# Kernel optimization log

Measured on AMD Instinct MI355X. Metric: run time of the kernel, lower is better.

## Reference

```python
import jax, jax.numpy as jnp
import numpy as np

H, CH = 4, 16          # heads, hidden_features // heads
SLOPE = 0.2            # leaky_relu negative slope


def gat(x, W, a_src, a_dst):
    # x: (B, N, C); W: (hidden, C); a_src/a_dst: (H, CH)
    B, N, _ = x.shape
    h = (x @ W.T).reshape(B, N, H, CH)
    a1 = jnp.einsum('bnhc,hc->bnh', h, a_src)   # att_src scores
    a2 = jnp.einsum('bnhc,hc->bnh', h, a_dst)   # att_dst scores
    # torch: a1.unsqueeze(1) + a2.unsqueeze(2) -> (B, N, N, H)
    e = a1[:, None, :, :] + a2[:, :, None, :]
    e = jnp.transpose(e, (0, 3, 1, 2))          # (B, H, N, N)
    e = jnp.where(e >= 0, e, SLOPE * e)         # leaky_relu
    return jax.nn.softmax(e, axis=2)            # softmax over dim=2 as in torch


def pool(x, W1, b1, W2, b2):
    # diff-pool assignment: (B, N, K), then x' = S^T x -> (B, K, C)
    s = jax.nn.softmax(jax.nn.relu(x @ W1.T + b1) @ W2.T + b2, axis=-1)
    return jnp.einsum('bnk,bnc->bkc', s, x)


def fuse(att0, atts, lefts, rights):
    out = att0
    for a, l, r in zip(atts, lefts, rights):
        # left (H,J0,K) @ att (B,H,K,K) @ right (H,K,J0), broadcast over batch
        out = out + jnp.einsum('hjk,bhkl,hlm->bhjm', l, a, r)
    return out


def setup_inputs() -> dict:
    key = jax.random.key(0)
    ks = iter(jax.random.split(key, 40))
    n = lambda shape, s=0.1: jax.random.normal(next(ks), shape, dtype=jnp.float32) * s
    inp = {
        'src': n((64, 64, 64, 25), 1.0),
        'gat_lin': n((6, 64, 64)), 'gat_asrc': n((6, 4, 16)), 'gat_adst': n((6, 4, 16)),
        'sp0_W1': n((64, 64)), 'sp0_b1': jnp.zeros((64,), jnp.float32),
        'sp0_W2': n((12, 64)), 'sp0_b2': jnp.zeros((12,), jnp.float32),
        'sp1_W1': n((64, 64)), 'sp1_b1': jnp.zeros((64,), jnp.float32),
        'sp1_W2': n((5, 64)), 'sp1_b2': jnp.zeros((5,), jnp.float32),
        'tp0_W1': n((64, 64)), 'tp0_b1': jnp.zeros((64,), jnp.float32),
        'tp0_W2': n((32, 64)), 'tp0_b2': jnp.zeros((32,), jnp.float32),
        'tp1_W1': n((64, 64)), 'tp1_b1': jnp.zeros((64,), jnp.float32),
        'tp1_W2': n((12, 64)), 'tp1_b2': jnp.zeros((12,), jnp.float32),
        'sl0': n((4, 25, 12)), 'sr0': n((4, 12, 25)),
        'sl1': n((4, 25, 5)), 'sr1': n((4, 5, 25)),
        'tl0': n((4, 64, 32)), 'tr0': n((4, 32, 64)),
        'tl1': n((4, 64, 12)), 'tr1': n((4, 12, 64)),
    }
    return inp


def reference(src, gat_lin, gat_asrc, gat_adst,
              sp0_W1, sp0_b1, sp0_W2, sp0_b2, sp1_W1, sp1_b1, sp1_W2, sp1_b2,
              tp0_W1, tp0_b1, tp0_W2, tp0_b2, tp1_W1, tp1_b1, tp1_W2, tp1_b2,
              sl0, sr0, sl1, sr1, tl0, tr0, tl1, tr1):
    B, C, T, J = src.shape
    # ---- spatial branch: attention over joints per (batch, frame) ----
    xs = jnp.transpose(src, (0, 2, 3, 1)).reshape(B * T, J, C)
    a_s0 = gat(xs, gat_lin[0], gat_asrc[0], gat_adst[0])            # (BT,H,25,25)
    xs1 = pool(xs, sp0_W1, sp0_b1, sp0_W2, sp0_b2)                  # (BT,12,C)
    a_s1 = gat(xs1, gat_lin[1], gat_asrc[1], gat_adst[1])           # (BT,H,12,12)
    xs2 = pool(xs1, sp1_W1, sp1_b1, sp1_W2, sp1_b2)                 # (BT,5,C)
    a_s2 = gat(xs2, gat_lin[2], gat_asrc[2], gat_adst[2])           # (BT,H,5,5)
    s_fused = fuse(a_s0, [a_s1, a_s2], [sl0, sl1], [sr0, sr1])
    # ---- temporal branch: attention over frames per (batch, joint) ----
    xt = jnp.transpose(src, (0, 3, 2, 1)).reshape(B * J, T, C)
    a_t0 = gat(xt, gat_lin[3], gat_asrc[3], gat_adst[3])            # (BJ,H,64,64)
    xt1 = pool(xt, tp0_W1, tp0_b1, tp0_W2, tp0_b2)                  # (BJ,32,C)
    a_t1 = gat(xt1, gat_lin[4], gat_asrc[4], gat_adst[4])
    xt2 = pool(xt1, tp1_W1, tp1_b1, tp1_W2, tp1_b2)                 # (BJ,12,C)
    a_t2 = gat(xt2, gat_lin[5], gat_asrc[5], gat_adst[5])
    t_fused = fuse(a_t0, [a_t1, a_t2], [tl0, tl1], [tr0, tr1])
    return (s_fused.reshape(B, T, H, J, J), t_fused.reshape(B, J, H, T, T))
```

## Files before the change

kernel.cpp:

```cpp
#include <hip/hip_runtime.h>

#define DEVINL __device__ __forceinline__

DEVINL float leaky(float v) { return v >= 0.f ? v : 0.2f * v; }

__global__ void wprep_kernel(const float* __restrict__ lin,
                             const float* __restrict__ asrc,
                             const float* __restrict__ adst,
                             float* __restrict__ w_out) {
    int idx = blockIdx.x * blockDim.x + threadIdx.x;
    if (idx >= 6 * 4 * 64) return;
    int c = idx & 63;
    int h = (idx >> 6) & 3;
    int k = idx >> 8;
    const float* L = lin + k * 64 * 64;
    float s1 = 0.f, s2 = 0.f;
    for (int e = 0; e < 16; ++e) {
        float w = L[(h * 16 + e) * 64 + c];
        s1 += w * asrc[(k * 4 + h) * 16 + e];
        s2 += w * adst[(k * 4 + h) * 16 + e];
    }
    w_out[(k * 2 + 0) * 256 + h * 64 + c] = s1;
    w_out[(k * 2 + 1) * 256 + h * 64 + c] = s2;
}

__global__ void wtrans_kernel(const float* __restrict__ s0, const float* __restrict__ s1,
                              const float* __restrict__ t0, const float* __restrict__ t1,
                              const float* __restrict__ s0w2, const float* __restrict__ s1w2,
                              const float* __restrict__ t0w2, const float* __restrict__ t1w2,
                              float* __restrict__ o) {
    int idx = blockIdx.x * 256 + threadIdx.x;
    if (idx < 16384) {
        int m = idx >> 12, r = idx & 4095, c = r >> 6, d = r & 63;
        const float* src = (m == 0) ? s0 : (m == 1) ? s1 : (m == 2) ? t0 : t1;
        o[idx] = src[d * 64 + c];
    } else if (idx < 16384 + 768) {
        int j = idx - 16384, c = j / 12, k = j - 12 * c;
        o[idx] = s0w2[k * 64 + c];
    } else if (idx < 17152 + 512) {
        int j = idx - 17152, c = j >> 3, k = j & 7;
        o[idx] = (k < 5) ? s1w2[k * 64 + c] : 0.f;
    } else if (idx < 17664 + 2048) {
        int j = idx - 17664, c = j >> 5, k = j & 31;
        o[idx] = t0w2[k * 64 + c];
    } else if (idx < 19712 + 768) {
        int j = idx - 19712, c = j / 12, k = j - 12 * c;
        o[idx] = t1w2[k * 64 + c];
    }
}

__global__ void xs_kernel(const float* __restrict__ src, float* __restrict__ xs) {
    int g = blockIdx.x;
    int b = g >> 6, t = g & 63;
    __shared__ float tile[64][26];
    const float* sp = src + b * 102400 + t * 25;
    for (int idx = threadIdx.x; idx < 64 * 25; idx += blockDim.x) {
        int c = idx / 25, j = idx - c * 25;
        tile[c][j] = sp[c * 1600 + j];
    }
    __syncthreads();
    float* op = xs + g * 25 * 64;
    for (int idx = threadIdx.x; idx < 25 * 64; idx += blockDim.x) {
        int j = idx >> 6, c = idx & 63;
        op[idx] = tile[c][j];
    }
}

__global__ void xt_kernel(const float* __restrict__ src, float* __restrict__ xt) {
    int g = blockIdx.x;
    int b = g / 25, j = g - b * 25;
    __shared__ float tile[64][65];
    const float* sp = src + b * 102400 + j;
    for (int idx = threadIdx.x; idx < 64 * 64; idx += blockDim.x) {
        int c = idx >> 6, t = idx & 63;
        tile[c][t] = sp[c * 1600 + t * 25];
    }
    __syncthreads();
    float* op = xt + g * 64 * 64;
    for (int idx = threadIdx.x; idx < 64 * 64; idx += blockDim.x) {
        int t = idx >> 6, c = idx & 63;
        op[idx] = tile[c][t];
    }
}

template <int N>
__global__ __launch_bounds__(256) void gat_kernel(
    const float* __restrict__ x,
    const float* __restrict__ w,
    float* __restrict__ att) {
    int g = blockIdx.x;
    const int tid = threadIdx.x;
    __shared__ float xlT[64][N + 1];
    __shared__ float wl[512];
    __shared__ float a1s[4 * N], a2s[4 * N];
    __shared__ float mxs[4];
    __shared__ float mjs[4 * N], invs[4 * N];
    const float* xp = x + (size_t)g * N * 64;
    for (int idx = tid; idx < N * 64; idx += 256) {
        int n = idx >> 6, c = idx & 63;
        xlT[c][n] = xp[idx];
    }
    for (int idx = tid; idx < 512; idx += 256) wl[idx] = w[idx];
    __syncthreads();
    for (int idx = tid; idx < 8 * N; idx += 256) {
        int n = idx % N;
        int hh = (idx / N) & 3;
        int sd = idx / (4 * N);
        const float* wp = wl + sd * 256 + hh * 64;
        float acc = 0.f;
        #pragma unroll 8
        for (int c = 0; c < 64; ++c) acc += xlT[c][n] * wp[c];
        (sd == 0 ? a1s : a2s)[hh * N + n] = acc;
    }
    __syncthreads();
    if (tid < 4) {
        float m = -1e30f;
        for (int i = 0; i < N; ++i) m = fmaxf(m, a2s[tid * N + i]);
        mxs[tid] = m;
    }
    __syncthreads();
    for (int idx = tid; idx < 4 * N; idx += 256) {
        int hh = idx / N;
        float aj = a1s[idx];
        float mj = leaky(aj + mxs[hh]);
        float ssum = 0.f;
        for (int i = 0; i < N; ++i) ssum += __expf(leaky(aj + a2s[hh * N + i]) - mj);
        mjs[idx] = mj;
        invs[idx] = 1.f / ssum;
    }
    __syncthreads();
    float* ob = att + (size_t)g * 4 * N * N;
    if constexpr ((N % 4) == 0) {
        constexpr int NF4 = N / 4;
        for (int idx = tid; idx < 4 * N * NF4; idx += 256) {
            int row = idx / NF4;
            int j0 = (idx - row * NF4) * 4;
            int hh = row / N, i = row - hh * N;
            float4 q1 = *(const float4*)&a1s[hh * N + j0];
            float4 qm = *(const float4*)&mjs[hh * N + j0];
            float4 qv = *(const float4*)&invs[hh * N + j0];
            float a2i = a2s[hh * N + i];
            float a1v[4] = {q1.x, q1.y, q1.z, q1.w};
            float mv[4] = {qm.x, qm.y, qm.z, qm.w};
            float iv[4] = {qv.x, qv.y, qv.z, qv.w};
            float r[4];
            #pragma unroll
            for (int c = 0; c < 4; ++c) {
                float e = a1v[c] + a2i;
                e = e >= 0.f ? e : 0.2f * e;
                r[c] = __expf(e - mv[c]) * iv[c];
            }
            *(float4*)&ob[row * N + j0] = make_float4(r[0], r[1], r[2], r[3]);
        }
    } else {
        for (int idx = tid; idx < 4 * N * N; idx += 256) {
            int hh = idx / (N * N), rem = idx - hh * N * N;
            int i = rem / N, j = rem - i * N;
            float e = a1s[hh * N + j] + a2s[hh * N + i];
            e = e >= 0.f ? e : 0.2f * e;
            ob[idx] = __expf(e - mjs[hh * N + j]) * invs[hh * N + j];
        }
    }
}

template <int N, int K, int KP>
__global__ __launch_bounds__(256, 3) void pool_kernel(
    const float* __restrict__ x,
    const float* __restrict__ W1T,
    const float* __restrict__ b1,
    const float* __restrict__ W2T,
    const float* __restrict__ b2,
    float* __restrict__ xo) {
    constexpr int NP = (N + 3) & ~3;
    constexpr int LDN = NP + 1;
    __shared__ float xlT[64 * LDN];
    __shared__ float yT[64 * LDN];
    __shared__ float sT[KP * LDN];
    const int g = blockIdx.x, tid = threadIdx.x;
    const float* xp = x + (size_t)g * N * 64;
    for (int i4 = tid; i4 < N * 16; i4 += 256) {
        int n = i4 >> 4, c0 = (i4 & 15) << 2;
        float4 v = ((const float4*)xp)[i4];
        xlT[(c0 + 0) * LDN + n] = v.x;
        xlT[(c0 + 1) * LDN + n] = v.y;
        xlT[(c0 + 2) * LDN + n] = v.z;
        xlT[(c0 + 3) * LDN + n] = v.w;
    }
    if constexpr (NP > N) {
        for (int i = tid; i < 64 * (NP - N); i += 256) {
            int c = i / (NP - N), n = N + i % (NP - N);
            xlT[c * LDN + n] = 0.f;
        }
    }
    __syncthreads();
    constexpr int T1 = (NP / 4) * 16;
    if (tid < T1) {
        int d0 = (tid & 15) << 2, n0 = (tid >> 4) << 2;
        float acc[4][4] = {};
        #pragma unroll 4
        for (int c = 0; c < 64; ++c) {
            float4 w4 = *(const float4*)(W1T + c * 64 + d0);
            float wv[4] = {w4.x, w4.y, w4.z, w4.w};
            float xv[4];
            #pragma unroll
            for (int r = 0; r < 4; ++r) xv[r] = xlT[c * LDN + n0 + r];
            #pragma unroll
            for (int r = 0; r < 4; ++r)
                #pragma unroll
                for (int cc = 0; cc < 4; ++cc) acc[r][cc] += xv[r] * wv[cc];
        }
        float4 b4 = *(const float4*)(b1 + d0);
        float bb[4] = {b4.x, b4.y, b4.z, b4.w};
        #pragma unroll
        for (int r = 0; r < 4; ++r)
            #pragma unroll
            for (int cc = 0; cc < 4; ++cc)
                yT[(d0 + cc) * LDN + n0 + r] = fmaxf(acc[r][cc] + bb[cc], 0.f);
    }
    __syncthreads();
    constexpr int KG4 = KP / 4;
    constexpr int T2 = (NP / 4) * KG4;
    if (tid < T2) {
        int k0 = (tid % KG4) << 2, n0 = (tid / KG4) << 2;
        float acc[4][4] = {};
        #pragma unroll 4
        for (int d = 0; d < 64; ++d) {
            float4 w4 = *(const float4*)(W2T + d * KP + k0);
            float wv[4] = {w4.x, w4.y, w4.z, w4.w};
            float yv[4];
            #pragma unroll
            for (int r = 0; r < 4; ++r) yv[r] = yT[d * LDN + n0 + r];
            #pragma unroll
            for (int r = 0; r < 4; ++r)
                #pragma unroll
                for (int cc = 0; cc < 4; ++cc) acc[r][cc] += yv[r] * wv[cc];
        }
        #pragma unroll
        for (int cc = 0; cc < 4; ++cc) {
            int k = k0 + cc;
            float bb = (k < K) ? b2[k] : 0.f;
            #pragma unroll
            for (int r = 0; r < 4; ++r)
                sT[k * LDN + n0 + r] = (k < K) ? (acc[r][cc] + bb) : -1e30f;
        }
    }
    __syncthreads();
    if (tid < NP) {
        float m = -1e30f;
        #pragma unroll
        for (int k = 0; k < KP; ++k) m = fmaxf(m, sT[k * LDN + tid]);
        float sum = 0.f;
        float e[KP];
        #pragma unroll
        for (int k = 0; k < KP; ++k) { e[k] = __expf(sT[k * LDN + tid] - m); sum += e[k]; }
        float inv = 1.f / sum;
        #pragma unroll
        for (int k = 0; k < KP; ++k) sT[k * LDN + tid] = e[k] * inv;
    }
    __syncthreads();
    constexpr int KG2 = (K + 1) / 2;
    constexpr int T3 = KG2 * 16;
    if (tid < T3) {
        int k0 = (tid % KG2) * 2, c0 = (tid / KG2) * 4;
        float acc0[4] = {}, acc1[4] = {};
        #pragma unroll 4
        for (int n = 0; n < N; ++n) {
            float sv0 = sT[k0 * LDN + n];
            float sv1 = sT[(k0 + 1) * LDN + n];
            float xv[4];
            #pragma unroll
            for (int j = 0; j < 4; ++j) xv[j] = xlT[(c0 + j) * LDN + n];
            #pragma unroll
            for (int j = 0; j < 4; ++j) { acc0[j] += sv0 * xv[j]; acc1[j] += sv1 * xv[j]; }
        }
        float* op = xo + (size_t)g * K * 64;
        *(float4*)&op[k0 * 64 + c0] = make_float4(acc0[0], acc0[1], acc0[2], acc0[3]);
        if (k0 + 1 < K)
            *(float4*)&op[(k0 + 1) * 64 + c0] = make_float4(acc1[0], acc1[1], acc1[2], acc1[3]);
    }
}

__global__ __launch_bounds__(256, 5) void gatfuse_t(
    const float* __restrict__ x,
    const float* __restrict__ w,
    const float* __restrict__ A1g,
    const float* __restrict__ L1,
    const float* __restrict__ R1,
    const float* __restrict__ A2g,
    const float* __restrict__ L2,
    const float* __restrict__ R2,
    float* __restrict__ out)
{
    const int bid = blockIdx.x;
    const int g = (bid & 7) | ((bid >> 5) << 3);
    const int h = (bid >> 3) & 3;
    const int tid = threadIdx.x;
    __shared__ float t1T[32 * 64];
    __shared__ float r1l[32 * 64];
    __shared__ float t2T[12 * 64];
    __shared__ float r2l[12 * 64];
    __shared__ float A1T[32 * 32];
    __shared__ float A2T[12 * 13];
    __shared__ float a1s[64], a2s[64], mjs[64], invs[64];

    if (tid < 128) {
        int t = tid & 63, sd = tid >> 6;
        const float4* xr = (const float4*)(x + (size_t)g * 4096 + t * 64);
        const float* wv = w + sd * 256 + h * 64;
        float acc = 0.f;
        #pragma unroll
        for (int q = 0; q < 16; ++q) {
            float4 xv = xr[q];
            acc += xv.x * wv[q * 4] + xv.y * wv[q * 4 + 1] +
                   xv.z * wv[q * 4 + 2] + xv.w * wv[q * 4 + 3];
        }
        (sd == 0 ? a1s : a2s)[t] = acc;
    } else {
        int u = tid - 128;
        const float* a1p = A1g + (size_t)(g * 4 + h) * 1024;
        #pragma unroll
        for (int q = 0; q < 8; ++q) {
            int idx = q * 128 + u;
            A1T[(idx & 31) * 32 + (idx >> 5)] = a1p[idx];
        }
        const float* a2p = A2g + (size_t)(g * 4 + h) * 144;
        for (int idx = u; idx < 144; idx += 128) {
            int k = idx / 12, l = idx - k * 12;
            A2T[l * 13 + k] = a2p[idx];
        }
        const float4* r1p = (const float4*)(R1 + h * 2048);
        #pragma unroll
        for (int q = 0; q < 4; ++q) ((float4*)r1l)[q * 128 + u] = r1p[q * 128 + u];
        const float4* r2p = (const float4*)(R2 + h * 768);
        for (int idx = u; idx < 192; idx += 128) ((float4*)r2l)[idx] = r2p[idx];
    }
    __syncthreads();

    if (tid < 64) {
        float mx = a2s[0];
        for (int i = 1; i < 64; ++i) mx = fmaxf(mx, a2s[i]);
        float aj = a1s[tid];
        float mj = leaky(aj + mx);
        float ssum = 0.f;
        for (int i = 0; i < 64; ++i) ssum += __expf(leaky(aj + a2s[i]) - mj);
        mjs[tid] = mj;
        invs[tid] = 1.f / ssum;
    }
    {
        int j = tid & 63, l0 = (tid >> 6) * 8;
        float lj[32];
        const float4* lp = (const float4*)(L1 + (h * 64 + j) * 32);
        #pragma unroll
        for (int q = 0; q < 8; ++q) {
            float4 v = lp[q];
            lj[q * 4] = v.x; lj[q * 4 + 1] = v.y; lj[q * 4 + 2] = v.z; lj[q * 4 + 3] = v.w;
        }
        for (int l = l0; l < l0 + 8; ++l) {
            const float* ar = &A1T[l * 32];
            float acc = 0.f;
            #pragma unroll
            for (int k = 0; k < 32; ++k) acc += lj[k] * ar[k];
            t1T[l * 64 + j] = acc;
        }
    }
    {
        int j = tid & 63, lb = (tid >> 6) * 3;
        float lj2[12];
        const float* lp2 = L2 + (h * 64 + j) * 12;
        #pragma unroll
        for (int k = 0; k < 12; ++k) lj2[k] = lp2[k];
        for (int l = lb; l < lb + 3; ++l) {
            const float* ar = &A2T[l * 13];
            float acc = 0.f;
            #pragma unroll
            for (int k = 0; k < 12; ++k) acc += lj2[k] * ar[k];
            t2T[l * 64 + j] = acc;
        }
    }
    __syncthreads();

    const int i0 = (tid >> 4) << 2, m0 = (tid & 15) << 2;
    float acc[4][4];
    {
        float4 q1 = *(const float4*)&a1s[m0];
        float4 qm = *(const float4*)&mjs[m0];
        float4 qv = *(const float4*)&invs[m0];
        float4 q2 = *(const float4*)&a2s[i0];
        float am[4] = {q1.x, q1.y, q1.z, q1.w};
        float mv[4] = {qm.x, qm.y, qm.z, qm.w};
        float iv[4] = {qv.x, qv.y, qv.z, qv.w};
        float ai[4] = {q2.x, q2.y, q2.z, q2.w};
        #pragma unroll
        for (int r = 0; r < 4; ++r)
            #pragma unroll
            for (int c = 0; c < 4; ++c) {
                float e = am[c] + ai[r];
                e = e >= 0.f ? e : 0.2f * e;
                acc[r][c] = __expf(e - mv[c]) * iv[c];
            }
    }
    #pragma unroll 8
    for (int l = 0; l < 32; ++l) {
        float4 t4 = *(const float4*)&t1T[l * 64 + i0];
        float4 r4 = *(const float4*)&r1l[l * 64 + m0];
        float tv[4] = {t4.x, t4.y, t4.z, t4.w};
        float rv[4] = {r4.x, r4.y, r4.z, r4.w};
        #pragma unroll
        for (int r = 0; r < 4; ++r)
            #pragma unroll
            for (int c = 0; c < 4; ++c) acc[r][c] += tv[r] * rv[c];
    }
    #pragma unroll 4
    for (int l = 0; l < 12; ++l) {
        float4 t4 = *(const float4*)&t2T[l * 64 + i0];
        float4 r4 = *(const float4*)&r2l[l * 64 + m0];
        float tv[4] = {t4.x, t4.y, t4.z, t4.w};
        float rv[4] = {r4.x, r4.y, r4.z, r4.w};
        #pragma unroll
        for (int r = 0; r < 4; ++r)
            #pragma unroll
            for (int c = 0; c < 4; ++c) acc[r][c] += tv[r] * rv[c];
    }
    float* op = out + (size_t)(g * 4 + h) * 4096;
    #pragma unroll
    for (int r = 0; r < 4; ++r)
        *(float4*)&op[(i0 + r) * 64 + m0] =
            make_float4(acc[r][0], acc[r][1], acc[r][2], acc[r][3]);
}

__global__ __launch_bounds__(256) void gatfuse_s(
    const float* __restrict__ x,
    const float* __restrict__ w,
    const float* __restrict__ A1g,
    const float* __restrict__ L1,
    const float* __restrict__ R1,
    const float* __restrict__ A2g,
    const float* __restrict__ L2,
    const float* __restrict__ R2,
    float* __restrict__ out)
{
    const int g = blockIdx.x;
    const int tid = threadIdx.x;
    const int h = tid >> 6, t = tid & 63;
    __shared__ float xl[25 * 68];
    __shared__ float A1T[4][12 * 12];
    __shared__ float A2T[4][5 * 5];
    __shared__ float t1l[4][25 * 12];
    __shared__ float t2l[4][25 * 5];
    __shared__ float r1l[4][12 * 25];
    __shared__ float r2l[4][5 * 25];
    __shared__ float a1s[4][25], a2s[4][25], mjs[4][32], invs[4][32];

    const float* xp = x + (size_t)g * 1600;
    for (int idx = tid; idx < 1600; idx += 256) {
        int n = idx >> 6, c = idx & 63;
        xl[n * 68 + c] = xp[idx];
    }
    const float* a1p = A1g + (size_t)(g * 4 + h) * 144;
    for (int idx = t; idx < 144; idx += 64) {
        int k = idx / 12, l = idx - k * 12;
        A1T[h][l * 12 + k] = a1p[idx];
    }
    const float* a2p = A2g + (size_t)(g * 4 + h) * 25;
    if (t < 25) {
        int k = t / 5, l = t - 5 * k;
        A2T[h][l * 5 + k] = a2p[t];
    }
    for (int idx = t; idx < 300; idx += 64) r1l[h][idx] = R1[h * 300 + idx];
    for (int idx = t; idx < 125; idx += 64) r2l[h][idx] = R2[h * 125 + idx];
    __syncthreads();

    if (t < 25) {
        const float* ws_ = w + h * 64;
        const float* wd_ = w + 256 + h * 64;
        const float* xr = &xl[t * 68];
        float s1 = 0.f, s2 = 0.f;
        #pragma unroll
        for (int c = 0; c < 64; c += 4) {
            float4 xv = *(const float4*)&xr[c];
            s1 += xv.x * ws_[c] + xv.y * ws_[c + 1] + xv.z * ws_[c + 2] + xv.w * ws_[c + 3];
            s2 += xv.x * wd_[c] + xv.y * wd_[c + 1] + xv.z * wd_[c + 2] + xv.w * wd_[c + 3];
        }
        a1s[h][t] = s1;
        a2s[h][t] = s2;
    }
    __syncthreads();

    if (t < 25) {
        float mx = a2s[h][0];
        for (int i = 1; i < 25; ++i) mx = fmaxf(mx, a2s[h][i]);
        float aj = a1s[h][t];
        float mj = leaky(aj + mx);
        float ssum = 0.f;
        for (int i = 0; i < 25; ++i) ssum += __expf(leaky(aj + a2s[h][i]) - mj);
        mjs[h][t] = mj;
        invs[h][t] = 1.f / ssum;
        float lj[12];
        const float* lp = L1 + (h * 25 + t) * 12;
        #pragma unroll
        for (int k = 0; k < 12; ++k) lj[k] = lp[k];
        #pragma unroll
        for (int l = 0; l < 12; ++l) {
            const float* ar = &A1T[h][l * 12];
            float acc = 0.f;
            #pragma unroll
            for (int k = 0; k < 12; ++k) acc += lj[k] * ar[k];
            t1l[h][t * 12 + l] = acc;
        }
        float lj2[5];
        const float* lp2 = L2 + (h * 25 + t) * 5;
        #pragma unroll
        for (int k = 0; k < 5; ++k) lj2[k] = lp2[k];
        #pragma unroll
        for (int l = 0; l < 5; ++l) {
            const float* ar = &A2T[h][l * 5];
            float acc = 0.f;
            #pragma unroll
            for (int k = 0; k < 5; ++k) acc += lj2[k] * ar[k];
            t2l[h][t * 5 + l] = acc;
        }
    }
    __syncthreads();

    float* op = out + (size_t)(g * 4 + h) * 625;
    for (int idx = t; idx < 625; idx += 64) {
        int i = idx / 25, m = idx - i * 25;
        float e = a1s[h][m] + a2s[h][i];
        e = e >= 0.f ? e : 0.2f * e;
        float val = __expf(e - mjs[h][m]) * invs[h][m];
        const float* t1r = &t1l[h][i * 12];
        const float* r1c = &r1l[h][m];
        #pragma unroll
        for (int l = 0; l < 12; ++l) val += t1r[l] * r1c[l * 25];
        const float* t2r = &t2l[h][i * 5];
        const float* r2c = &r2l[h][m];
        #pragma unroll
        for (int l = 0; l < 5; ++l) val += t2r[l] * r2c[l * 25];
        op[idx] = val;
    }
}

extern "C" void kernel_launch(void* const* d_in, const int* in_sizes, int n_in,
                              void* d_out, int out_size, void* d_ws, size_t ws_size,
                              hipStream_t stream) {
    const float* src    = (const float*)d_in[0];
    const float* lin    = (const float*)d_in[1];
    const float* asrc   = (const float*)d_in[2];
    const float* adst   = (const float*)d_in[3];
    const float* sp0_W1 = (const float*)d_in[4];
    const float* sp0_b1 = (const float*)d_in[5];
    const float* sp0_W2 = (const float*)d_in[6];
    const float* sp0_b2 = (const float*)d_in[7];
    const float* sp1_W1 = (const float*)d_in[8];
    const float* sp1_b1 = (const float*)d_in[9];
    const float* sp1_W2 = (const float*)d_in[10];
    const float* sp1_b2 = (const float*)d_in[11];
    const float* tp0_W1 = (const float*)d_in[12];
    const float* tp0_b1 = (const float*)d_in[13];
    const float* tp0_W2 = (const float*)d_in[14];
    const float* tp0_b2 = (const float*)d_in[15];
    const float* tp1_W1 = (const float*)d_in[16];
    const float* tp1_b1 = (const float*)d_in[17];
    const float* tp1_W2 = (const float*)d_in[18];
    const float* tp1_b2 = (const float*)d_in[19];
    const float* sl0    = (const float*)d_in[20];
    const float* sr0    = (const float*)d_in[21];
    const float* sl1    = (const float*)d_in[22];
    const float* sr1    = (const float*)d_in[23];
    const float* tl0    = (const float*)d_in[24];
    const float* tr0    = (const float*)d_in[25];
    const float* tl1    = (const float*)d_in[26];
    const float* tr1    = (const float*)d_in[27];

    float* out_s = (float*)d_out;
    float* out_t = out_s + 10240000;

    float* ws     = (float*)d_ws;
    float* wbuf   = ws;
    float* wT     = ws + 4096;
    float* region = ws + 24576;

    float* sp0_W1T = wT;
    float* sp1_W1T = wT + 4096;
    float* tp0_W1T = wT + 8192;
    float* tp1_W1T = wT + 12288;
    float* sp0_W2T = wT + 16384;
    float* sp1_W2T = wT + 17152;
    float* tp0_W2T = wT + 17664;
    float* tp1_W2T = wT + 19712;

    float* xs  = region;
    float* xs1 = xs + 6553600;
    float* xs2 = xs1 + 3145728;
    float* as1 = xs2 + 1310720;
    float* as2 = as1 + 2359296;
    float* xt  = region;
    float* xt1 = xt + 6553600;
    float* xt2 = xt1 + 3276800;
    float* at1 = xt2 + 1228800;
    float* at2 = at1 + 6553600;

    wprep_kernel<<<6, 256, 0, stream>>>(lin, asrc, adst, wbuf);
    wtrans_kernel<<<80, 256, 0, stream>>>(sp0_W1, sp1_W1, tp0_W1, tp1_W1,
                                          sp0_W2, sp1_W2, tp0_W2, tp1_W2, wT);

    xs_kernel<<<4096, 256, 0, stream>>>(src, xs);
    pool_kernel<25, 12, 12><<<4096, 256, 0, stream>>>(xs, sp0_W1T, sp0_b1, sp0_W2T, sp0_b2, xs1);
    gat_kernel<12><<<4096, 256, 0, stream>>>(xs1, wbuf + 1 * 512, as1);
    pool_kernel<12, 5, 8><<<4096, 256, 0, stream>>>(xs1, sp1_W1T, sp1_b1, sp1_W2T, sp1_b2, xs2);
    gat_kernel<5><<<4096, 256, 0, stream>>>(xs2, wbuf + 2 * 512, as2);
    gatfuse_s<<<4096, 256, 0, stream>>>(xs, wbuf + 0 * 512, as1, sl0, sr0, as2, sl1, sr1, out_s);

    xt_kernel<<<1600, 256, 0, stream>>>(src, xt);
    pool_kernel<64, 32, 32><<<1600, 256, 0, stream>>>(xt, tp0_W1T, tp0_b1, tp0_W2T, tp0_b2, xt1);
    gat_kernel<32><<<1600, 256, 0, stream>>>(xt1, wbuf + 4 * 512, at1);
    pool_kernel<32, 12, 12><<<1600, 256, 0, stream>>>(xt1, tp1_W1T, tp1_b1, tp1_W2T, tp1_b2, xt2);
    gat_kernel<12><<<1600, 256, 0, stream>>>(xt2, wbuf + 5 * 512, at2);
    gatfuse_t<<<6400, 256, 0, stream>>>(xt, wbuf + 3 * 512, at1, tl0, tr0, at2, tl1, tr1, out_t);
}
```

Measured before the change: 360.2 us.

## Store only GAT scores and recompute attention softmax inside fuse kernels

Replaces the per-level gat kernels, which wrote full (H,N,N) attention matrices to global memory, with a batched score kernel that writes only the 8 per-node score vectors. The fuse kernels now rebuild the softmaxed attention matrices for all three levels from these scores in shared memory. This removes large intermediate attention writes and reads (several MB per level) at the cost of recomputing exps in the fuse kernels. It also reads R1/R2 directly from global memory in gatfuse_t, pads layouts for float4 dot products in gatfuse_s, and raises occupancy hints.

```diff
diff --git a/kernel.cpp b/kernel.cpp
--- a/kernel.cpp
+++ b/kernel.cpp
@@ -83,83 +83,35 @@
     }
 }
 
-template <int N>
-__global__ __launch_bounds__(256) void gat_kernel(
+template <int N, int GPB>
+__global__ __launch_bounds__(256) void score_kernel(
     const float* __restrict__ x,
     const float* __restrict__ w,
-    float* __restrict__ att) {
-    int g = blockIdx.x;
+    float* __restrict__ sc) {
+    constexpr int NP = GPB * N;
+    constexpr int LD = NP + 1;
+    __shared__ float xlT[64 * LD];
+    __shared__ float wl[512];
+    const int g0 = blockIdx.x * GPB;
     const int tid = threadIdx.x;
-    __shared__ float xlT[64][N + 1];
-    __shared__ float wl[512];
-    __shared__ float a1s[4 * N], a2s[4 * N];
-    __shared__ float mxs[4];
-    __shared__ float mjs[4 * N], invs[4 * N];
-    const float* xp = x + (size_t)g * N * 64;
-    for (int idx = tid; idx < N * 64; idx += 256) {
+    const float* xp = x + (size_t)g0 * N * 64;
+    for (int idx = tid; idx < NP * 64; idx += 256) {
         int n = idx >> 6, c = idx & 63;
-        xlT[c][n] = xp[idx];
+        xlT[c * LD + n] = xp[idx];
     }
     for (int idx = tid; idx < 512; idx += 256) wl[idx] = w[idx];
     __syncthreads();
-    for (int idx = tid; idx < 8 * N; idx += 256) {
+    float* op = sc + (size_t)g0 * 8 * N;
+    for (int idx = tid; idx < 8 * NP; idx += 256) {
         int n = idx % N;
-        int hh = (idx / N) & 3;
-        int sd = idx / (4 * N);
-        const float* wp = wl + sd * 256 + hh * 64;
+        int q = (idx / N) & 7;
+        int gs = idx / (8 * N);
+        int nn = gs * N + n;
+        const float* wp = wl + q * 64;
         float acc = 0.f;
         #pragma unroll 8
-        for (int c = 0; c < 64; ++c) acc += xlT[c][n] * wp[c];
-        (sd == 0 ? a1s : a2s)[hh * N + n] = acc;
-    }
-    __syncthreads();
-    if (tid < 4) {
-        float m = -1e30f;
-        for (int i = 0; i < N; ++i) m = fmaxf(m, a2s[tid * N + i]);
-        mxs[tid] = m;
-    }
-    __syncthreads();
-    for (int idx = tid; idx < 4 * N; idx += 256) {
-        int hh = idx / N;
-        float aj = a1s[idx];
-        float mj = leaky(aj + mxs[hh]);
-        float ssum = 0.f;
-        for (int i = 0; i < N; ++i) ssum += __expf(leaky(aj + a2s[hh * N + i]) - mj);
-        mjs[idx] = mj;
-        invs[idx] = 1.f / ssum;
-    }
-    __syncthreads();
-    float* ob = att + (size_t)g * 4 * N * N;
-    if constexpr ((N % 4) == 0) {
-        constexpr int NF4 = N / 4;
-        for (int idx = tid; idx < 4 * N * NF4; idx += 256) {
-            int row = idx / NF4;
-            int j0 = (idx - row * NF4) * 4;
-            int hh = row / N, i = row - hh * N;
-            float4 q1 = *(const float4*)&a1s[hh * N + j0];
-            float4 qm = *(const float4*)&mjs[hh * N + j0];
-            float4 qv = *(const float4*)&invs[hh * N + j0];
-            float a2i = a2s[hh * N + i];
-            float a1v[4] = {q1.x, q1.y, q1.z, q1.w};
-            float mv[4] = {qm.x, qm.y, qm.z, qm.w};
-            float iv[4] = {qv.x, qv.y, qv.z, qv.w};
-            float r[4];
-            #pragma unroll
-            for (int c = 0; c < 4; ++c) {
-                float e = a1v[c] + a2i;
-                e = e >= 0.f ? e : 0.2f * e;
-                r[c] = __expf(e - mv[c]) * iv[c];
-            }
-            *(float4*)&ob[row * N + j0] = make_float4(r[0], r[1], r[2], r[3]);
-        }
-    } else {
-        for (int idx = tid; idx < 4 * N * N; idx += 256) {
-            int hh = idx / (N * N), rem = idx - hh * N * N;
-            int i = rem / N, j = rem - i * N;
-            float e = a1s[hh * N + j] + a2s[hh * N + i];
-            e = e >= 0.f ? e : 0.2f * e;
-            ob[idx] = __expf(e - mjs[hh * N + j]) * invs[hh * N + j];
-        }
+        for (int c = 0; c < 64; ++c) acc += xlT[c * LD + nn] * wp[c];
+        op[idx] = acc;
     }
 }
 
@@ -280,13 +232,12 @@
     }
 }
 
-__global__ __launch_bounds__(256, 5) void gatfuse_t(
-    const float* __restrict__ x,
-    const float* __restrict__ w,
-    const float* __restrict__ A1g,
+__global__ __launch_bounds__(256, 8) void gatfuse_t(
+    const float* __restrict__ sc0,
+    const float* __restrict__ sc1,
+    const float* __restrict__ sc2,
     const float* __restrict__ L1,
     const float* __restrict__ R1,
-    const float* __restrict__ A2g,
     const float* __restrict__ L2,
     const float* __restrict__ R2,
     float* __restrict__ out)
@@ -296,84 +247,98 @@
     const int h = (bid >> 3) & 3;
     const int tid = threadIdx.x;
     __shared__ float t1T[32 * 64];
-    __shared__ float r1l[32 * 64];
     __shared__ float t2T[12 * 64];
-    __shared__ float r2l[12 * 64];
-    __shared__ float A1T[32 * 32];
-    __shared__ float A2T[12 * 13];
-    __shared__ float a1s[64], a2s[64], mjs[64], invs[64];
+    __shared__ float A1[32 * 36];
+    __shared__ float A2[12 * 13];
+    __shared__ float a01[64], a02[64], mj0[64], iv0[64];
+    __shared__ float a11[32], a12[32], mj1[32], iv1[32];
+    __shared__ float a21[12], a22[12], mj2[12], iv2[12];
 
     if (tid < 128) {
         int t = tid & 63, sd = tid >> 6;
-        const float4* xr = (const float4*)(x + (size_t)g * 4096 + t * 64);
-        const float* wv = w + sd * 256 + h * 64;
-        float acc = 0.f;
-        #pragma unroll
-        for (int q = 0; q < 16; ++q) {
-            float4 xv = xr[q];
-            acc += xv.x * wv[q * 4] + xv.y * wv[q * 4 + 1] +
-                   xv.z * wv[q * 4 + 2] + xv.w * wv[q * 4 + 3];
-        }
-        (sd == 0 ? a1s : a2s)[t] = acc;
-    } else {
-        int u = tid - 128;
-        const float* a1p = A1g + (size_t)(g * 4 + h) * 1024;
-        #pragma unroll
-        for (int q = 0; q < 8; ++q) {
-            int idx = q * 128 + u;
-            A1T[(idx & 31) * 32 + (idx >> 5)] = a1p[idx];
-        }
-        const float* a2p = A2g + (size_t)(g * 4 + h) * 144;
-        for (int idx = u; idx < 144; idx += 128) {
-            int k = idx / 12, l = idx - k * 12;
-            A2T[l * 13 + k] = a2p[idx];
-        }
-        const float4* r1p = (const float4*)(R1 + h * 2048);
-        #pragma unroll
-        for (int q = 0; q < 4; ++q) ((float4*)r1l)[q * 128 + u] = r1p[q * 128 + u];
-        const float4* r2p = (const float4*)(R2 + h * 768);
-        for (int idx = u; idx < 192; idx += 128) ((float4*)r2l)[idx] = r2p[idx];
+        (sd ? a02 : a01)[t] = sc0[((size_t)g * 8 + sd * 4 + h) * 64 + t];
+    } else if (tid < 192) {
+        int u = tid - 128, sd = u >> 5, n = u & 31;
+        (sd ? a12 : a11)[n] = sc1[((size_t)g * 8 + sd * 4 + h) * 32 + n];
+    } else if (tid < 216) {
+        int u = tid - 192, sd = u / 12, n = u - sd * 12;
+        (sd ? a22 : a21)[n] = sc2[((size_t)g * 8 + sd * 4 + h) * 12 + n];
     }
     __syncthreads();
 
     if (tid < 64) {
-        float mx = a2s[0];
-        for (int i = 1; i < 64; ++i) mx = fmaxf(mx, a2s[i]);
-        float aj = a1s[tid];
+        float mx = a02[0];
+        for (int i = 1; i < 64; ++i) mx = fmaxf(mx, a02[i]);
+        float aj = a01[tid];
         float mj = leaky(aj + mx);
-        float ssum = 0.f;
-        for (int i = 0; i < 64; ++i) ssum += __expf(leaky(aj + a2s[i]) - mj);
-        mjs[tid] = mj;
-        invs[tid] = 1.f / ssum;
-    }
+        float s = 0.f;
+        for (int i = 0; i < 64; ++i) s += __expf(leaky(aj + a02[i]) - mj);
+        mj0[tid] = mj; iv0[tid] = 1.f / s;
+    } else if (tid < 96) {
+        int l = tid - 64;
+        float mx = a12[0];
+        for (int k = 1; k < 32; ++k) mx = fmaxf(mx, a12[k]);
+        float aj = a11[l];
+        float mj = leaky(aj + mx);
+        float s = 0.f;
+        for (int k = 0; k < 32; ++k) s += __expf(leaky(aj + a12[k]) - mj);
+        mj1[l] = mj; iv1[l] = 1.f / s;
+    } else if (tid < 108) {
+        int l = tid - 96;
+        float mx = a22[0];
+        for (int k = 1; k < 12; ++k) mx = fmaxf(mx, a22[k]);
+        float aj = a21[l];
+        float mj = leaky(aj + mx);
+        float s = 0.f;
+        for (int k = 0; k < 12; ++k) s += __expf(leaky(aj + a22[k]) - mj);
+        mj2[l] = mj; iv2[l] = 1.f / s;
+    }
+    __syncthreads();
+
+    #pragma unroll
+    for (int q = 0; q < 4; ++q) {
+        int idx = q * 256 + tid;
+        int k = idx >> 5, l = idx & 31;
+        float e = leaky(a11[l] + a12[k]);
+        A1[k * 36 + l] = __expf(e - mj1[l]) * iv1[l];
+    }
+    if (tid < 144) {
+        int k = tid / 12, l = tid - k * 12;
+        float e = leaky(a21[l] + a22[k]);
+        A2[k * 13 + l] = __expf(e - mj2[l]) * iv2[l];
+    }
+    __syncthreads();
+
     {
-        int j = tid & 63, l0 = (tid >> 6) * 8;
-        float lj[32];
-        const float4* lp = (const float4*)(L1 + (h * 64 + j) * 32);
-        #pragma unroll
-        for (int q = 0; q < 8; ++q) {
-            float4 v = lp[q];
-            lj[q * 4] = v.x; lj[q * 4 + 1] = v.y; lj[q * 4 + 2] = v.z; lj[q * 4 + 3] = v.w;
-        }
-        for (int l = l0; l < l0 + 8; ++l) {
-            const float* ar = &A1T[l * 32];
+        const int j = tid & 63, l0 = (tid >> 6) * 8;
+        const float* ljrow = L1 + ((size_t)h * 64 + j) * 32;
+        float acc8[8] = {};
+        for (int k = 0; k < 32; ++k) {
+            float lk = ljrow[k];
+            float4 a4a = *(const float4*)&A1[k * 36 + l0];
+            float4 a4b = *(const float4*)&A1[k * 36 + l0 + 4];
+            acc8[0] += lk * a4a.x; acc8[1] += lk * a4a.y;
+            acc8[2] += lk * a4a.z; acc8[3] += lk * a4a.w;
+            acc8[4] += lk * a4b.x; acc8[5] += lk * a4b.y;
+            acc8[6] += lk * a4b.z; acc8[7] += lk * a4b.w;
+        }
+        #pragma unroll
+        for (int lo = 0; lo < 8; ++lo) t1T[(l0 + lo) * 64 + j] = acc8[lo];
+        const int lb = (tid >> 6) * 3;
+        float lj2[12];
+        const float4* lp2 = (const float4*)(L2 + ((size_t)h * 64 + j) * 12);
+        #pragma unroll
+        for (int q = 0; q < 3; ++q) {
+            float4 v = lp2[q];
+            lj2[q * 4] = v.x; lj2[q * 4 + 1] = v.y;
+            lj2[q * 4 + 2] = v.z; lj2[q * 4 + 3] = v.w;
+        }
+        #pragma unroll
+        for (int lo = 0; lo < 3; ++lo) {
+            int l = lb + lo;
             float acc = 0.f;
             #pragma unroll
-            for (int k = 0; k < 32; ++k) acc += lj[k] * ar[k];
-            t1T[l * 64 + j] = acc;
-        }
-    }
-    {
-        int j = tid & 63, lb = (tid >> 6) * 3;
-        float lj2[12];
-        const float* lp2 = L2 + (h * 64 + j) * 12;
-        #pragma unroll
-        for (int k = 0; k < 12; ++k) lj2[k] = lp2[k];
-        for (int l = lb; l < lb + 3; ++l) {
-            const float* ar = &A2T[l * 13];
-            float acc = 0.f;
-            #pragma unroll
-            for (int k = 0; k < 12; ++k) acc += lj2[k] * ar[k];
+            for (int k = 0; k < 12; ++k) acc += lj2[k] * A2[k * 13 + l];
             t2T[l * 64 + j] = acc;
         }
     }
@@ -382,10 +347,10 @@
     const int i0 = (tid >> 4) << 2, m0 = (tid & 15) << 2;
     float acc[4][4];
     {
-        float4 q1 = *(const float4*)&a1s[m0];
-        float4 qm = *(const float4*)&mjs[m0];
-        float4 qv = *(const float4*)&invs[m0];
-        float4 q2 = *(const float4*)&a2s[i0];
+        float4 q1 = *(const float4*)&a01[m0];
+        float4 qm = *(const float4*)&mj0[m0];
+        float4 qv = *(const float4*)&iv0[m0];
+        float4 q2 = *(const float4*)&a02[i0];
         float am[4] = {q1.x, q1.y, q1.z, q1.w};
         float mv[4] = {qm.x, qm.y, qm.z, qm.w};
         float iv[4] = {qv.x, qv.y, qv.z, qv.w};
@@ -399,10 +364,11 @@
                 acc[r][c] = __expf(e - mv[c]) * iv[c];
             }
     }
+    const float* r1b = R1 + (size_t)h * 2048;
     #pragma unroll 8
     for (int l = 0; l < 32; ++l) {
         float4 t4 = *(const float4*)&t1T[l * 64 + i0];
-        float4 r4 = *(const float4*)&r1l[l * 64 + m0];
+        float4 r4 = *(const float4*)(r1b + l * 64 + m0);
         float tv[4] = {t4.x, t4.y, t4.z, t4.w};
         float rv[4] = {r4.x, r4.y, r4.z, r4.w};
         #pragma unroll
@@ -410,10 +376,11 @@
             #pragma unroll
             for (int c = 0; c < 4; ++c) acc[r][c] += tv[r] * rv[c];
     }
+    const float* r2b = R2 + (size_t)h * 768;
     #pragma unroll 4
     for (int l = 0; l < 12; ++l) {
         float4 t4 = *(const float4*)&t2T[l * 64 + i0];
-        float4 r4 = *(const float4*)&r2l[l * 64 + m0];
+        float4 r4 = *(const float4*)(r2b + l * 64 + m0);
         float tv[4] = {t4.x, t4.y, t4.z, t4.w};
         float rv[4] = {r4.x, r4.y, r4.z, r4.w};
         #pragma unroll
@@ -421,20 +388,19 @@
             #pragma unroll
             for (int c = 0; c < 4; ++c) acc[r][c] += tv[r] * rv[c];
     }
-    float* op = out + (size_t)(g * 4 + h) * 4096;
+    float* op = out + ((size_t)g * 4 + h) * 4096;
     #pragma unroll
     for (int r = 0; r < 4; ++r)
         *(float4*)&op[(i0 + r) * 64 + m0] =
             make_float4(acc[r][0], acc[r][1], acc[r][2], acc[r][3]);
 }
 
-__global__ __launch_bounds__(256) void gatfuse_s(
-    const float* __restrict__ x,
-    const float* __restrict__ w,
-    const float* __restrict__ A1g,
+__global__ __launch_bounds__(256, 6) void gatfuse_s(
+    const float* __restrict__ sc0,
+    const float* __restrict__ sc1,
+    const float* __restrict__ sc2,
     const float* __restrict__ L1,
     const float* __restrict__ R1,
-    const float* __restrict__ A2g,
     const float* __restrict__ L2,
     const float* __restrict__ R2,
     float* __restrict__ out)
@@ -442,100 +408,136 @@
     const int g = blockIdx.x;
     const int tid = threadIdx.x;
     const int h = tid >> 6, t = tid & 63;
-    __shared__ float xl[25 * 68];
-    __shared__ float A1T[4][12 * 12];
-    __shared__ float A2T[4][5 * 5];
-    __shared__ float t1l[4][25 * 12];
-    __shared__ float t2l[4][25 * 5];
-    __shared__ float r1l[4][12 * 25];
-    __shared__ float r2l[4][5 * 25];
-    __shared__ float a1s[4][25], a2s[4][25], mjs[4][32], invs[4][32];
-
-    const float* xp = x + (size_t)g * 1600;
-    for (int idx = tid; idx < 1600; idx += 256) {
-        int n = idx >> 6, c = idx & 63;
-        xl[n * 68 + c] = xp[idx];
-    }
-    const float* a1p = A1g + (size_t)(g * 4 + h) * 144;
+    __shared__ float A1[4][12 * 13];
+    __shared__ float A2[4][5 * 6];
+    __shared__ float t1l[4][25 * 16];
+    __shared__ float t2l[4][25 * 8];
+    __shared__ float r1T[4][25 * 16];
+    __shared__ float r2T[4][25 * 8];
+    __shared__ float a01[4][25], a02[4][25], mj0[4][25], iv0[4][25];
+    __shared__ float a11[4][12], a12[4][12], mj1[4][12], iv1[4][12];
+    __shared__ float a21[4][5], a22[4][5], mj2[4][5], iv2[4][5];
+
+    if (t < 50) {
+        int sd = t / 25, n = t - sd * 25;
+        (sd ? a02[h] : a01[h])[n] = sc0[((size_t)g * 8 + sd * 4 + h) * 25 + n];
+    }
+    if (t < 24) {
+        int sd = t / 12, n = t - sd * 12;
+        (sd ? a12[h] : a11[h])[n] = sc1[((size_t)g * 8 + sd * 4 + h) * 12 + n];
+    }
+    if (t < 10) {
+        int sd = t / 5, n = t - sd * 5;
+        (sd ? a22[h] : a21[h])[n] = sc2[((size_t)g * 8 + sd * 4 + h) * 5 + n];
+    }
+    for (int idx = t; idx < 400; idx += 64) {
+        int m = idx >> 4, l = idx & 15;
+        r1T[h][idx] = (l < 12) ? R1[h * 300 + l * 25 + m] : 0.f;
+    }
+    for (int idx = t; idx < 200; idx += 64) {
+        int m = idx >> 3, l = idx & 7;
+        r2T[h][idx] = (l < 5) ? R2[h * 125 + l * 25 + m] : 0.f;
+    }
+    __syncthreads();
+
+    if (t < 25) {
+        float mx = a02[h][0];
+        for (int i = 1; i < 25; ++i) mx = fmaxf(mx, a02[h][i]);
+        float aj = a01[h][t];
+        float mj = leaky(aj + mx);
+        float s = 0.f;
+        for (int i = 0; i < 25; ++i) s += __expf(leaky(aj + a02[h][i]) - mj);
+        mj0[h][t] = mj; iv0[h][t] = 1.f / s;
+    }
+    if (t >= 32 && t < 44) {
+        int l = t - 32;
+        float mx = a12[h][0];
+        for (int k = 1; k < 12; ++k) mx = fmaxf(mx, a12[h][k]);
+        float aj = a11[h][l];
+        float mj = leaky(aj + mx);
+        float s = 0.f;
+        for (int k = 0; k < 12; ++k) s += __expf(leaky(aj + a12[h][k]) - mj);
+        mj1[h][l] = mj; iv1[h][l] = 1.f / s;
+    }
+    if (t >= 48 && t < 53) {
+        int l = t - 48;
+        float mx = a22[h][0];
+        for (int k = 1; k < 5; ++k) mx = fmaxf(mx, a22[h][k]);
+        float aj = a21[h][l];
+        float mj = leaky(aj + mx);
+        float s = 0.f;
+        for (int k = 0; k < 5; ++k) s += __expf(leaky(aj + a22[h][k]) - mj);
+        mj2[h][l] = mj; iv2[h][l] = 1.f / s;
+    }
+    __syncthreads();
+
     for (int idx = t; idx < 144; idx += 64) {
         int k = idx / 12, l = idx - k * 12;
-        A1T[h][l * 12 + k] = a1p[idx];
-    }
-    const float* a2p = A2g + (size_t)(g * 4 + h) * 25;
+        float e = leaky(a11[h][l] + a12[h][k]);
+        A1[h][k * 13 + l] = __expf(e - mj1[h][l]) * iv1[h][l];
+    }
     if (t < 25) {
-        int k = t / 5, l = t - 5 * k;
-        A2T[h][l * 5 + k] = a2p[t];
-    }
-    for (int idx = t; idx < 300; idx += 64) r1l[h][idx] = R1[h * 300 + idx];
-    for (int idx = t; idx < 125; idx += 64) r2l[h][idx] = R2[h * 125 + idx];
+        int k = t / 5, l = t - (t / 5) * 5;
+        float e = leaky(a21[h][l] + a22[h][k]);
+        A2[h][k * 6 + l] = __expf(e - mj2[h][l]) * iv2[h][l];
+    }
     __syncthreads();
 
     if (t < 25) {
-        const float* ws_ = w + h * 64;
-        const float* wd_ = w + 256 + h * 64;
-        const float* xr = &xl[t * 68];
-        float s1 = 0.f, s2 = 0.f;
-        #pragma unroll
-        for (int c = 0; c < 64; c += 4) {
-            float4 xv = *(const float4*)&xr[c];
-            s1 += xv.x * ws_[c] + xv.y * ws_[c + 1] + xv.z * ws_[c + 2] + xv.w * ws_[c + 3];
-            s2 += xv.x * wd_[c] + xv.y * wd_[c + 1] + xv.z * wd_[c + 2] + xv.w * wd_[c + 3];
-        }
-        a1s[h][t] = s1;
-        a2s[h][t] = s2;
-    }
-    __syncthreads();
-
-    if (t < 25) {
-        float mx = a2s[h][0];
-        for (int i = 1; i < 25; ++i) mx = fmaxf(mx, a2s[h][i]);
-        float aj = a1s[h][t];
-        float mj = leaky(aj + mx);
-        float ssum = 0.f;
-        for (int i = 0; i < 25; ++i) ssum += __expf(leaky(aj + a2s[h][i]) - mj);
-        mjs[h][t] = mj;
-        invs[h][t] = 1.f / ssum;
         float lj[12];
-        const float* lp = L1 + (h * 25 + t) * 12;
-        #pragma unroll
-        for (int k = 0; k < 12; ++k) lj[k] = lp[k];
+        const float4* lp = (const float4*)(L1 + ((size_t)h * 25 + t) * 12);
+        #pragma unroll
+        for (int q = 0; q < 3; ++q) {
+            float4 v = lp[q];
+            lj[q * 4] = v.x; lj[q * 4 + 1] = v.y; lj[q * 4 + 2] = v.z; lj[q * 4 + 3] = v.w;
+        }
         #pragma unroll
         for (int l = 0; l < 12; ++l) {
-            const float* ar = &A1T[h][l * 12];
             float acc = 0.f;
             #pragma unroll
-            for (int k = 0; k < 12; ++k) acc += lj[k] * ar[k];
-            t1l[h][t * 12 + l] = acc;
-        }
+            for (int k = 0; k < 12; ++k) acc += lj[k] * A1[h][k * 13 + l];
+            t1l[h][t * 16 + l] = acc;
+        }
+        #pragma unroll
+        for (int l = 12; l < 16; ++l) t1l[h][t * 16 + l] = 0.f;
         float lj2[5];
-        const float* lp2 = L2 + (h * 25 + t) * 5;
+        const float* lp2 = L2 + ((size_t)h * 25 + t) * 5;
         #pragma unroll
         for (int k = 0; k < 5; ++k) lj2[k] = lp2[k];
         #pragma unroll
         for (int l = 0; l < 5; ++l) {
-            const float* ar = &A2T[h][l * 5];
             float acc = 0.f;
             #pragma unroll
-            for (int k = 0; k < 5; ++k) acc += lj2[k] * ar[k];
-            t2l[h][t * 5 + l] = acc;
-        }
-    }
-    __syncthreads();
-
-    float* op = out + (size_t)(g * 4 + h) * 625;
+            for (int k = 0; k < 5; ++k) acc += lj2[k] * A2[h][k * 6 + l];
+            t2l[h][t * 8 + l] = acc;
+        }
+        #pragma unroll
+        for (int l = 5; l < 8; ++l) t2l[h][t * 8 + l] = 0.f;
+    }
+    __syncthreads();
+
+    float* op = out + ((size_t)g * 4 + h) * 625;
     for (int idx = t; idx < 625; idx += 64) {
         int i = idx / 25, m = idx - i * 25;
-        float e = a1s[h][m] + a2s[h][i];
+        float e = a01[h][m] + a02[h][i];
         e = e >= 0.f ? e : 0.2f * e;
-        float val = __expf(e - mjs[h][m]) * invs[h][m];
-        const float* t1r = &t1l[h][i * 12];
-        const float* r1c = &r1l[h][m];
-        #pragma unroll
-        for (int l = 0; l < 12; ++l) val += t1r[l] * r1c[l * 25];
-        const float* t2r = &t2l[h][i * 5];
-        const float* r2c = &r2l[h][m];
-        #pragma unroll
-        for (int l = 0; l < 5; ++l) val += t2r[l] * r2c[l * 25];
+        float val = __expf(e - mj0[h][m]) * iv0[h][m];
+        const float* t1r = &t1l[h][i * 16];
+        const float* r1c = &r1T[h][m * 16];
+        #pragma unroll
+        for (int q = 0; q < 4; ++q) {
+            float4 tv = *(const float4*)&t1r[q * 4];
+            float4 rv = *(const float4*)&r1c[q * 4];
+            val += tv.x * rv.x + tv.y * rv.y + tv.z * rv.z + tv.w * rv.w;
+        }
+        const float* t2r = &t2l[h][i * 8];
+        const float* r2c = &r2T[h][m * 8];
+        #pragma unroll
+        for (int q = 0; q < 2; ++q) {
+            float4 tv = *(const float4*)&t2r[q * 4];
+            float4 rv = *(const float4*)&r2c[q * 4];
+            val += tv.x * rv.x + tv.y * rv.y + tv.z * rv.z + tv.w * rv.w;
+        }
         op[idx] = val;
     }
 }
@@ -575,10 +577,10 @@
     float* out_s = (float*)d_out;
     float* out_t = out_s + 10240000;
 
-    float* ws     = (float*)d_ws;
-    float* wbuf   = ws;
-    float* wT     = ws + 4096;
-    float* region = ws + 24576;
+    float* ws   = (float*)d_ws;
+    float* wbuf = ws;
+    float* wT   = ws + 4096;
+    float* base = ws + 24576;
 
     float* sp0_W1T = wT;
     float* sp1_W1T = wT + 4096;
@@ -589,32 +591,37 @@
     float* tp0_W2T = wT + 17664;
     float* tp1_W2T = wT + 19712;
 
-    float* xs  = region;
-    float* xs1 = xs + 6553600;
-    float* xs2 = xs1 + 3145728;
-    float* as1 = xs2 + 1310720;
-    float* as2 = as1 + 2359296;
-    float* xt  = region;
-    float* xt1 = xt + 6553600;
-    float* xt2 = xt1 + 3276800;
-    float* at1 = xt2 + 1228800;
-    float* at2 = at1 + 6553600;
+    float* xs  = base;
+    float* xs1 = base + 6553600;
+    float* xs2 = base + 9699328;
+    float* xt  = base;
+    float* xt1 = base + 6553600;
+    float* xt2 = base + 9830400;
+    float* scb = base + 11059200;
+    float* scS0 = scb;
+    float* scS1 = scb + 819200;
+    float* scS2 = scb + 1212416;
+    float* scT0 = scb;
+    float* scT1 = scb + 819200;
+    float* scT2 = scb + 1228800;
 
     wprep_kernel<<<6, 256, 0, stream>>>(lin, asrc, adst, wbuf);
     wtrans_kernel<<<80, 256, 0, stream>>>(sp0_W1, sp1_W1, tp0_W1, tp1_W1,
                                           sp0_W2, sp1_W2, tp0_W2, tp1_W2, wT);
 
     xs_kernel<<<4096, 256, 0, stream>>>(src, xs);
+    score_kernel<25, 2><<<2048, 256, 0, stream>>>(xs, wbuf + 0 * 512, scS0);
     pool_kernel<25, 12, 12><<<4096, 256, 0, stream>>>(xs, sp0_W1T, sp0_b1, sp0_W2T, sp0_b2, xs1);
-    gat_kernel<12><<<4096, 256, 0, stream>>>(xs1, wbuf + 1 * 512, as1);
+    score_kernel<12, 4><<<1024, 256, 0, stream>>>(xs1, wbuf + 1 * 512, scS1);
     pool_kernel<12, 5, 8><<<4096, 256, 0, stream>>>(xs1, sp1_W1T, sp1_b1, sp1_W2T, sp1_b2, xs2);
-    gat_kernel<5><<<4096, 256, 0, stream>>>(xs2, wbuf + 2 * 512, as2);
-    gatfuse_s<<<4096, 256, 0, stream>>>(xs, wbuf + 0 * 512, as1, sl0, sr0, as2, sl1, sr1, out_s);
+    score_kernel<5, 8><<<512, 256, 0, stream>>>(xs2, wbuf + 2 * 512, scS2);
+    gatfuse_s<<<4096, 256, 0, stream>>>(scS0, scS1, scS2, sl0, sr0, sl1, sr1, out_s);
 
     xt_kernel<<<1600, 256, 0, stream>>>(src, xt);
+    score_kernel<64, 1><<<1600, 256, 0, stream>>>(xt, wbuf + 3 * 512, scT0);
     pool_kernel<64, 32, 32><<<1600, 256, 0, stream>>>(xt, tp0_W1T, tp0_b1, tp0_W2T, tp0_b2, xt1);
-    gat_kernel<32><<<1600, 256, 0, stream>>>(xt1, wbuf + 4 * 512, at1);
+    score_kernel<32, 2><<<800, 256, 0, stream>>>(xt1, wbuf + 4 * 512, scT1);
     pool_kernel<32, 12, 12><<<1600, 256, 0, stream>>>(xt1, tp1_W1T, tp1_b1, tp1_W2T, tp1_b2, xt2);
-    gat_kernel<12><<<1600, 256, 0, stream>>>(xt2, wbuf + 5 * 512, at2);
-    gatfuse_t<<<6400, 256, 0, stream>>>(xt, wbuf + 3 * 512, at1, tl0, tr0, at2, tl1, tr1, out_t);
-}
+    score_kernel<12, 4><<<400, 256, 0, stream>>>(xt2, wbuf + 5 * 512, scT2);
+    gatfuse_t<<<6400, 256, 0, stream>>>(scT0, scT1, scT2, tl0, tr0, tl1, tr1, out_t);
+}
```

Result: slower. 386.8 us (+7.4%).
